# Kernel optimization log

Measured on AMD Instinct MI355X. Metric: run time of the kernel, lower is better.

The kernel has to match this reference:

```python
import jax, jax.numpy as jnp
import numpy as np

N_QUBITS = 14
N_LAYERS = 5
N_ACTIONS = 2
BETA = 1.0
BATCH = 2048
DIM = 2 ** N_QUBITS

# static diagonal sign tables (wire 0 = most significant bit)
_idx = np.arange(DIM)

def _bit(q):
    return (_idx >> (N_QUBITS - 1 - q)) & 1

# CZ ring: all CZ gates are diagonal and commute -> fold into one sign vector
_pairs = [(i, i + 1) for i in range(N_QUBITS - 1)] + ([(N_QUBITS - 1, 0)] if N_QUBITS > 2 else [])
_ring = np.ones(DIM, np.float32)
for _q1, _q2 in _pairs:
    _ring *= np.where((_bit(_q1) & _bit(_q2)) == 1, -1.0, 1.0).astype(np.float32)
RING_SIGN = jnp.asarray(_ring)
# Z tensor Z ... tensor Z eigenvalues: parity of bitstring
_zz = np.where(np.array([bin(i).count('1') for i in range(DIM)]) % 2 == 1, -1.0, 1.0).astype(np.float32)
ZZ_SIGN = jnp.asarray(_zz)


def _rx(t):
    c = jnp.cos(t / 2).astype(jnp.complex64)
    s = (-1j) * jnp.sin(t / 2).astype(jnp.complex64)
    return jnp.stack([jnp.stack([c, s], -1), jnp.stack([s, c], -1)], -2)


def _ry(t):
    c = jnp.cos(t / 2).astype(jnp.complex64)
    s = jnp.sin(t / 2).astype(jnp.complex64)
    return jnp.stack([jnp.stack([c, -s], -1), jnp.stack([s, c], -1)], -2)


def _rz(t):
    em = jnp.exp(-1j * t / 2).astype(jnp.complex64)
    ep = jnp.exp(1j * t / 2).astype(jnp.complex64)
    z = jnp.zeros_like(em)
    return jnp.stack([jnp.stack([em, z], -1), jnp.stack([z, ep], -1)], -2)


def _apply_1q(state, U, q):
    # state: (B, 2^n) complex64; U: (2,2) shared or (B,2,2) per-sample
    B = state.shape[0]
    s = state.reshape(B, 2 ** q, 2, 2 ** (N_QUBITS - q - 1))
    if U.ndim == 2:
        s = jnp.einsum('ij,bljr->blir', U, s)
    else:
        s = jnp.einsum('bij,bljr->blir', U, s)
    return s.reshape(B, DIM)


def _circuit(theta, inp):
    # inp: (B, N_LAYERS * N_QUBITS) encoding angles; returns (B, 1) expval of Z^n
    B = inp.shape[0]
    state = jnp.zeros((B, DIM), jnp.complex64).at[:, 0].set(1.0)
    vi = 0
    for l in range(N_LAYERS + 1):
        ang = theta[vi:vi + 3 * N_QUBITS].reshape(N_QUBITS, 3)
        vi += 3 * N_QUBITS
        for q in range(N_QUBITS):
            # Rx then Ry then Rz fused into one 2x2 unitary
            U = _rz(ang[q, 2]) @ _ry(ang[q, 1]) @ _rx(ang[q, 0])
            state = _apply_1q(state, U, q)
        if l < N_LAYERS:
            state = state * RING_SIGN  # CZ entangling ring
            enc = inp[:, l * N_QUBITS:(l + 1) * N_QUBITS]
            for q in range(N_QUBITS):
                state = _apply_1q(state, _rx(enc[:, q]), q)
    p = state.real ** 2 + state.imag ** 2
    return jnp.sum(p * ZZ_SIGN, axis=1, keepdims=True)


def setup_inputs() -> dict:
    key = jax.random.key(0)
    k1, k2 = jax.random.split(key, 2)
    x = jax.random.normal(k1, (BATCH, N_QUBITS), jnp.float32)
    theta = jax.random.uniform(k2, (3 * N_QUBITS * (N_LAYERS + 1),), jnp.float32) * np.float32(np.pi)
    lam = jnp.ones((N_QUBITS * N_LAYERS,), jnp.float32)
    # Alternating output layer init: [[1, -1, 1, ...]]
    w = jnp.asarray([[(-1.0) ** i for i in range(N_ACTIONS)]], jnp.float32)
    return {"x": x, "theta": theta, "lam": lam, "w": w}


def reference(x, theta, lam, w):
    inp = jnp.tile(x, (1, N_LAYERS)) * lam          # (B, L*n)
    vals = _circuit(theta, inp)                      # (B, 1)
    logits = (vals @ w) * BETA                       # (B, n_actions)
    return jax.nn.softmax(logits, axis=1)
```

## Files before the change

kernel.cpp:

```cpp
#include <hip/hip_runtime.h>
#include <math.h>

#define NQ        14
#define DIM       16384
#define NLAYERS   5
#define NTHREADS  512

typedef float vf2 __attribute__((ext_vector_type(2)));
struct c32 { float x, y; };

__host__ __device__ constexpr int lswz(int i) {
    return i ^ ((i >> 4) & 15) ^ ((i >> 8) & 15) ^ ((i >> 12) & 3);
}
__host__ __device__ constexpr unsigned sjc(int j) {
    return (((j >> 4) & (j >> 3)) ^ ((j >> 3) & (j >> 2)) ^
            ((j >> 2) & (j >> 1)) ^ ((j >> 1) & j)) & 1u;
}
__host__ __device__ constexpr unsigned pjc(int j) {
    return (((j >> 3) & (j >> 2)) ^ ((j >> 2) & (j >> 1)) ^ ((j >> 1) & j)) & 1u;
}

__device__ __forceinline__ c32 cmul(c32 a, c32 b) {
    return { a.x * b.x - a.y * b.y, a.x * b.y + a.y * b.x };
}
__device__ __forceinline__ vf2 sxor(vf2 v, unsigned m) {
    return vf2{ __uint_as_float(__float_as_uint(v.x) ^ m),
                __uint_as_float(__float_as_uint(v.y) ^ m) };
}

__device__ __forceinline__ vf2 cmulv(vf2 g, vf2 z) {
    vf2 o;
    asm("v_pk_mul_f32 %0, %1, %2 op_sel:[1,1] op_sel_hi:[1,0] neg_lo:[0,1] neg_hi:[0,0]\n\t"
        "v_pk_fma_f32 %0, %1, %2, %0 op_sel:[0,0,0] op_sel_hi:[0,1,1]"
        : "=&v"(o) : "v"(g), "v"(z));
    return o;
}

__device__ __forceinline__ void bfr(vf2 r, vf2& A0, vf2& A1) {
    vf2 b0, b1;
    asm("v_pk_mul_f32 %0, %2, %3 op_sel:[0,0] op_sel_hi:[0,1]\n\t"
        "v_pk_fma_f32 %0, %2, %4, %0 op_sel:[1,0,0] op_sel_hi:[1,1,1] neg_lo:[1,0,0] neg_hi:[1,0,0]\n\t"
        "v_pk_mul_f32 %1, %2, %3 op_sel:[1,0] op_sel_hi:[1,1]\n\t"
        "v_pk_fma_f32 %1, %2, %4, %1 op_sel:[0,0,0] op_sel_hi:[0,1,1]"
        : "=&v"(b0), "=&v"(b1)
        : "v"(r), "v"(A0), "v"(A1));
    A0 = b0; A1 = b1;
}

#define APPLY32R(K, RV) { const vf2 rv_ = (RV); _Pragma("unroll") \
    for (int mm = 0; mm < 16; ++mm) { \
        const int r0 = ((mm >> (K)) << ((K) + 1)) | (mm & ((1 << (K)) - 1)); \
        bfr(rv_, a[r0], a[r0 | (1 << (K))]); } }
#define APPLY16R(K, RV) { const vf2 rv_ = (RV); _Pragma("unroll") \
    for (int mm = 0; mm < 8; ++mm) { \
        const int r0 = ((mm >> (K)) << ((K) + 1)) | (mm & ((1 << (K)) - 1)); \
        bfr(rv_, aa[r0], aa[r0 | (1 << (K))]); } }

#define AMASK(j) ((((j) & 1) ? (((j) & 16) ? M11 : M10) : (((j) & 16) ? M01 : M00)) \
                  ^ (sjc(j) << 31))
#define CMASK(v, j) ((((v)) ? (((j) & 8) ? C11 : C10) : (((j) & 8) ? C01 : C00)) \
                     ^ (((pjc(j) ^ ((j) & (v) & 1)) & 1u) << 31))

__device__ __forceinline__ void passB(char* stb, const vf2* GrL, const vf2* Tk, int base2) {
    vf2 a[32];
    #pragma unroll
    for (int j = 0; j < 32; ++j)
        a[j] = *(const vf2*)(stb + (base2 ^ (lswz(j << 4) << 3)));
    #pragma unroll
    for (int j = 0; j < 32; ++j) a[j] = cmulv(Tk[j], a[j]);
    APPLY32R(4, GrL[5]); APPLY32R(3, GrL[6]); APPLY32R(2, GrL[7]);
    APPLY32R(1, GrL[8]); APPLY32R(0, GrL[9]);
    #pragma unroll
    for (int j = 0; j < 32; ++j)
        *(vf2*)(stb + (base2 ^ (lswz(j << 4) << 3))) = a[j];
}

__device__ __forceinline__ void passAA(char* stb, const vf2* GrA, const vf2* GrB,
                                       const vf2* Ta, const vf2* Tb, int base1,
                                       unsigned M00, unsigned M01, unsigned M10, unsigned M11) {
    vf2 a[32];
    #pragma unroll
    for (int j = 0; j < 32; ++j)
        a[j] = *(const vf2*)(stb + (base1 ^ (lswz(j << 9) << 3)));
    #pragma unroll
    for (int j = 0; j < 32; ++j) a[j] = cmulv(Ta[j], a[j]);
    APPLY32R(4, GrA[0]); APPLY32R(3, GrA[1]); APPLY32R(2, GrA[2]);
    APPLY32R(1, GrA[3]); APPLY32R(0, GrA[4]);
    #pragma unroll
    for (int j = 0; j < 32; ++j) a[j] = cmulv(Tb[j], sxor(a[j], AMASK(j)));
    APPLY32R(4, GrB[0]); APPLY32R(3, GrB[1]); APPLY32R(2, GrB[2]);
    APPLY32R(1, GrB[3]); APPLY32R(0, GrB[4]);
    #pragma unroll
    for (int j = 0; j < 32; ++j)
        *(vf2*)(stb + (base1 ^ (lswz(j << 9) << 3))) = a[j];
}

__device__ __forceinline__ void passCC(char* stb, const vf2* GrA, const vf2* GrB,
                                       const vf2* Ta, const vf2* Tb, int base3,
                                       unsigned C00, unsigned C01, unsigned C10, unsigned C11) {
    #pragma unroll
    for (int v = 0; v < 2; ++v) {
        const int bb = base3 ^ (lswz(v << 13) << 3);
        vf2 aa[16];
        #pragma unroll
        for (int j = 0; j < 16; ++j)
            aa[j] = *(const vf2*)(stb + (bb ^ (j << 3)));
        #pragma unroll
        for (int j = 0; j < 16; ++j) aa[j] = cmulv(Ta[j], aa[j]);
        APPLY16R(3, GrA[10]); APPLY16R(2, GrA[11]); APPLY16R(1, GrA[12]); APPLY16R(0, GrA[13]);
        #pragma unroll
        for (int j = 0; j < 16; ++j) aa[j] = cmulv(Tb[j], sxor(aa[j], CMASK(v, j)));
        APPLY16R(3, GrB[10]); APPLY16R(2, GrB[11]); APPLY16R(1, GrB[12]); APPLY16R(0, GrB[13]);
        #pragma unroll
        for (int j = 0; j < 16; ++j)
            *(vf2*)(stb + (bb ^ (j << 3))) = aa[j];
    }
}

__device__ __forceinline__ void passCLast(char* stb, const vf2* GrL, const vf2* Tk,
                                          int base3, float& se, float& so) {
    #pragma unroll
    for (int v = 0; v < 2; ++v) {
        const int bb = base3 ^ (lswz(v << 13) << 3);
        vf2 aa[16];
        #pragma unroll
        for (int j = 0; j < 16; ++j)
            aa[j] = *(const vf2*)(stb + (bb ^ (j << 3)));
        #pragma unroll
        for (int j = 0; j < 16; ++j) aa[j] = cmulv(Tk[j], aa[j]);
        APPLY16R(3, GrL[10]); APPLY16R(2, GrL[11]); APPLY16R(1, GrL[12]); APPLY16R(0, GrL[13]);
        #pragma unroll
        for (int j = 0; j < 16; ++j) {
            const float d = fmaf(aa[j].x, aa[j].x, aa[j].y * aa[j].y);
            if (((v ^ __popc(j)) & 1) == 0) se += d; else so += d;
        }
    }
}

__attribute__((amdgpu_flat_work_group_size(NTHREADS, NTHREADS),
               amdgpu_waves_per_eu(2, 2)))
__global__ void pqc_kernel(
    const float* __restrict__ x,
    const float* __restrict__ theta,
    const float* __restrict__ lam,
    const float* __restrict__ w,
    float* __restrict__ out)
{
    __shared__ vf2 st[DIM];
    __shared__ vf2 Gr[NLAYERS + 1][NQ];
    __shared__ vf2 Gang[NLAYERS + 1][NQ];
    __shared__ vf2 G0c[NQ][2];
    __shared__ vf2 F0[5][2];
    __shared__ vf2 T[15][32];
    __shared__ float wsum[NTHREADS / 64];

    const int t = threadIdx.x;
    const int b = blockIdx.x;
    char* stb = (char*)st;

    if (t < (NLAYERS + 1) * NQ) {
        const int l = t / NQ, q = t % NQ;
        const float a0 = theta[3 * t + 0];
        const float a1 = theta[3 * t + 1];
        const float a2t = theta[3 * t + 2];
        const float cx = cosf(0.5f * a0), sx = sinf(0.5f * a0);
        const float cy = cosf(0.5f * a1), sy = sinf(0.5f * a1);
        const float cz = cosf(0.5f * a2t), sz = sinf(0.5f * a2t);
        const c32 m00 = {  cy * cx,  sy * sx };
        const c32 m01 = { -sy * cx, -cy * sx };
        const c32 m10 = {  sy * cx, -cy * sx };
        c32 u00 = { cz * m00.x + sz * m00.y,  cz * m00.y - sz * m00.x };
        c32 u01 = { cz * m01.x + sz * m01.y,  cz * m01.y - sz * m01.x };
        c32 u10 = { cz * m10.x - sz * m10.y,  cz * m10.y + sz * m10.x };
        if (l >= 1) {
            const float ang = x[b * NQ + q] * lam[(l - 1) * NQ + q];
            const float c = cosf(0.5f * ang), s = sinf(0.5f * ang);
            const c32 u11 = { u00.x, -u00.y };
            const c32 v00 = { u00.x * c + s * u01.y,  u00.y * c - s * u01.x };
            const c32 v10 = { u10.x * c + s * u11.y,  u10.y * c - s * u11.x };
            u00 = v00; u10 = v10;
        }
        if (l == 0) {
            G0c[q][0] = vf2{ u00.x, u00.y };
            G0c[q][1] = vf2{ u10.x, u10.y };
        }
        const float cb = sqrtf(u00.x * u00.x + u00.y * u00.y);
        const float sb = sqrtf(u10.x * u10.x + u10.y * u10.y);
        const float inv = rsqrtf(fmaxf(cb * cb + sb * sb, 1e-30f));
        const float p  = atan2f(u00.y, u00.x);
        const float qq = atan2f(u10.y, u10.x);
        Gr[l][q]   = vf2{ cb * inv, sb * inv };
        Gang[l][q] = vf2{ 0.5f * (qq - p), -0.5f * (p + qq) };
    }
    __syncthreads();

    if (t < 448) {
        const int k = 1 + (t >> 5), j = t & 31;
        const int r = k % 6;
        const int win = (r == 0 || r == 5) ? 0 : ((r == 1 || r == 4) ? 1 : 2);
        if (win != 2 || j < 16) {
            const int lc = 1 + k / 3;
            const int lp = (k >= 3) ? lc - 1 : 0;
            const int nb = (win == 2) ? 4 : 5;
            float th = 0.f;
            for (int m = 0; m < nb; ++m) {
                const int q = (win == 0) ? (4 - m) : (win == 1) ? (9 - m) : (13 - m);
                float ww = Gang[lc][q].y;
                if (lp) ww += Gang[lp][q].x;
                th += ((j >> m) & 1) ? ww : -ww;
            }
            float sn, cn;
            __sincosf(th, &sn, &cn);
            T[k][j] = vf2{ cn, sn };
        }
    } else if (t < 458) {
        const int u = t - 448, q = u >> 1, be = u & 1;
        const float c2 = Gang[1][q].y;
        const float ph = be ? c2 : -c2;
        float sn, cn;
        __sincosf(ph, &sn, &cn);
        const vf2 g = G0c[q][be];
        const c32 f = cmul(c32{ g.x, g.y }, c32{ cn, sn });
        F0[q][be] = vf2{ f.x, f.y };
    }
    __syncthreads();

    const int base1 = lswz(t) << 3;
    const int base2 = lswz(((t & 0x1F0) << 5) | (t & 15)) << 3;
    const int base3 = lswz(t << 4) << 3;
    const unsigned Pp  = (unsigned)(__popc(t & (t >> 1) & 0xFF) & 1);
    const unsigned t8 = (t >> 8) & 1u, tb0 = t & 1u;
    const unsigned M00 =  Pp              << 31;
    const unsigned M10 = (Pp ^ t8)        << 31;
    const unsigned M01 = (Pp ^ tb0)       << 31;
    const unsigned M11 = (Pp ^ t8 ^ tb0)  << 31;
    const unsigned C00 =  Pp              << 31;
    const unsigned C01 = (Pp ^ tb0)       << 31;
    const unsigned C10 = (Pp ^ t8)        << 31;
    const unsigned C11 = (Pp ^ t8 ^ tb0)  << 31;

    {
        c32 pref = { G0c[5][(t >> 8) & 1].x, G0c[5][(t >> 8) & 1].y };
        #pragma unroll
        for (int qq = 6; qq <= 13; ++qq) {
            const vf2 g = G0c[qq][(t >> (13 - qq)) & 1];
            pref = cmul(pref, c32{ g.x, g.y });
        }
        c32 p01p[4], p234[8];
        #pragma unroll
        for (int k = 0; k < 4; ++k) {
            const vf2 ga = F0[0][k >> 1], gb = F0[1][k & 1];
            p01p[k] = cmul(pref, cmul(c32{ ga.x, ga.y }, c32{ gb.x, gb.y }));
        }
        #pragma unroll
        for (int m = 0; m < 8; ++m) {
            const vf2 g2 = F0[2][m >> 2], g3 = F0[3][(m >> 1) & 1], g4 = F0[4][m & 1];
            p234[m] = cmul(cmul(c32{ g2.x, g2.y }, c32{ g3.x, g3.y }), c32{ g4.x, g4.y });
        }
        vf2 a[32];
        #pragma unroll
        for (int j = 0; j < 32; ++j) {
            const c32 av = cmul(p01p[j >> 3], p234[j & 7]);
            a[j] = sxor(vf2{ av.x, av.y }, AMASK(j));
        }
        APPLY32R(4, Gr[1][0]); APPLY32R(3, Gr[1][1]); APPLY32R(2, Gr[1][2]);
        APPLY32R(1, Gr[1][3]); APPLY32R(0, Gr[1][4]);
        #pragma unroll
        for (int j = 0; j < 32; ++j)
            *(vf2*)(stb + (base1 ^ (lswz(j << 9) << 3))) = a[j];
    }
    __syncthreads();

    passB(stb, Gr[1], T[1], base2);                                        __syncthreads();
    passCC(stb, Gr[1], Gr[2], T[2], T[3], base3, C00, C01, C10, C11);      __syncthreads();
    passB(stb, Gr[2], T[4], base2);                                        __syncthreads();
    passAA(stb, Gr[2], Gr[3], T[5], T[6], base1, M00, M01, M10, M11);      __syncthreads();
    passB(stb, Gr[3], T[7], base2);                                        __syncthreads();
    passCC(stb, Gr[3], Gr[4], T[8], T[9], base3, C00, C01, C10, C11);      __syncthreads();
    passB(stb, Gr[4], T[10], base2);                                       __syncthreads();
    passAA(stb, Gr[4], Gr[5], T[11], T[12], base1, M00, M01, M10, M11);    __syncthreads();
    passB(stb, Gr[5], T[13], base2);                                       __syncthreads();
    float se = 0.f, so = 0.f;
    passCLast(stb, Gr[5], T[14], base3, se, so);

    float local = (__popc(t) & 1) ? (so - se) : (se - so);
    #pragma unroll
    for (int off = 32; off > 0; off >>= 1)
        local += __shfl_down(local, off, 64);
    if ((t & 63) == 0) wsum[t >> 6] = local;
    __syncthreads();
    if (t == 0) {
        float v = 0.0f;
        #pragma unroll
        for (int i = 0; i < NTHREADS / 64; ++i) v += wsum[i];
        const float BETA = 1.0f;
        const float l0 = v * w[0] * BETA, l1 = v * w[1] * BETA;
        const float m  = fmaxf(l0, l1);
        const float e0 = __expf(l0 - m), e1 = __expf(l1 - m);
        const float inv = 1.0f / (e0 + e1);
        out[2 * b + 0] = e0 * inv;
        out[2 * b + 1] = e1 * inv;
    }
}

extern "C" void kernel_launch(void* const* d_in, const int* in_sizes, int n_in,
                              void* d_out, int out_size, void* d_ws, size_t ws_size,
                              hipStream_t stream) {
    const float* x     = (const float*)d_in[0];
    const float* theta = (const float*)d_in[1];
    const float* lam   = (const float*)d_in[2];
    const float* w     = (const float*)d_in[3];
    float* out = (float*)d_out;
    const int batch = in_sizes[0] / NQ;
    pqc_kernel<<<batch, NTHREADS, 0, stream>>>(x, theta, lam, w, out);
}
```

Measured before the change: 291.1 us.

## Store LDS statevector in fp16 pairs to halve shared memory and raise occupancy

Stores the 16384-amplitude complex state in shared memory as packed half2 (4 bytes per amplitude) instead of float2, converting to and from fp32 around each pass. The bank swizzle is reworked for 4-byte elements, and waves_per_eu rises from 2 to 4, since halving LDS (128KB to 64KB) allows more blocks per CU. The aim is less LDS traffic and better latency hiding. The cost is fp16 rounding on every pass across many gate layers, which risks accuracy, plus extra conversion instructions and tighter register limits at the higher occupancy.

New measurement: 263.0 us (median of 2 runs). 1.11x faster.

```diff
diff --git a/kernel.cpp b/kernel.cpp
--- a/kernel.cpp
+++ b/kernel.cpp
@@ -1,4 +1,5 @@
 #include <hip/hip_runtime.h>
+#include <hip/hip_fp16.h>
 #include <math.h>
 
 #define NQ        14
@@ -9,8 +10,8 @@
 typedef float vf2 __attribute__((ext_vector_type(2)));
 struct c32 { float x, y; };
 
-__host__ __device__ constexpr int lswz(int i) {
-    return i ^ ((i >> 4) & 15) ^ ((i >> 8) & 15) ^ ((i >> 12) & 3);
+__host__ __device__ constexpr int lswz5(int i) {
+    return i ^ ((i >> 5) & 31) ^ ((i >> 10) & 15);
 }
 __host__ __device__ constexpr unsigned sjc(int j) {
     return (((j >> 4) & (j >> 3)) ^ ((j >> 3) & (j >> 2)) ^
@@ -26,6 +27,16 @@
 __device__ __forceinline__ vf2 sxor(vf2 v, unsigned m) {
     return vf2{ __uint_as_float(__float_as_uint(v.x) ^ m),
                 __uint_as_float(__float_as_uint(v.y) ^ m) };
+}
+
+__device__ __forceinline__ unsigned pk16(vf2 v) {
+    __half2 h = __float22half2_rn(float2{ v.x, v.y });
+    return *reinterpret_cast<unsigned*>(&h);
+}
+__device__ __forceinline__ vf2 up16(unsigned u) {
+    __half2 h = *reinterpret_cast<__half2*>(&u);
+    float2 f = __half22float2(h);
+    return vf2{ f.x, f.y };
 }
 
 __device__ __forceinline__ vf2 cmulv(vf2 g, vf2 z) {
@@ -65,14 +76,14 @@
     vf2 a[32];
     #pragma unroll
     for (int j = 0; j < 32; ++j)
-        a[j] = *(const vf2*)(stb + (base2 ^ (lswz(j << 4) << 3)));
+        a[j] = up16(*(const unsigned*)(stb + (base2 ^ (lswz5(j << 4) << 2))));
     #pragma unroll
     for (int j = 0; j < 32; ++j) a[j] = cmulv(Tk[j], a[j]);
     APPLY32R(4, GrL[5]); APPLY32R(3, GrL[6]); APPLY32R(2, GrL[7]);
     APPLY32R(1, GrL[8]); APPLY32R(0, GrL[9]);
     #pragma unroll
     for (int j = 0; j < 32; ++j)
-        *(vf2*)(stb + (base2 ^ (lswz(j << 4) << 3))) = a[j];
+        *(unsigned*)(stb + (base2 ^ (lswz5(j << 4) << 2))) = pk16(a[j]);
 }
 
 __device__ __forceinline__ void passAA(char* stb, const vf2* GrA, const vf2* GrB,
@@ -81,7 +92,7 @@
     vf2 a[32];
     #pragma unroll
     for (int j = 0; j < 32; ++j)
-        a[j] = *(const vf2*)(stb + (base1 ^ (lswz(j << 9) << 3)));
+        a[j] = up16(*(const unsigned*)(stb + (base1 ^ (lswz5(j << 9) << 2))));
     #pragma unroll
     for (int j = 0; j < 32; ++j) a[j] = cmulv(Ta[j], a[j]);
     APPLY32R(4, GrA[0]); APPLY32R(3, GrA[1]); APPLY32R(2, GrA[2]);
@@ -92,7 +103,7 @@
     APPLY32R(1, GrB[3]); APPLY32R(0, GrB[4]);
     #pragma unroll
     for (int j = 0; j < 32; ++j)
-        *(vf2*)(stb + (base1 ^ (lswz(j << 9) << 3))) = a[j];
+        *(unsigned*)(stb + (base1 ^ (lswz5(j << 9) << 2))) = pk16(a[j]);
 }
 
 __device__ __forceinline__ void passCC(char* stb, const vf2* GrA, const vf2* GrB,
@@ -100,11 +111,11 @@
                                        unsigned C00, unsigned C01, unsigned C10, unsigned C11) {
     #pragma unroll
     for (int v = 0; v < 2; ++v) {
-        const int bb = base3 ^ (lswz(v << 13) << 3);
+        const int bb = base3 ^ (lswz5(v << 13) << 2);
         vf2 aa[16];
         #pragma unroll
         for (int j = 0; j < 16; ++j)
-            aa[j] = *(const vf2*)(stb + (bb ^ (j << 3)));
+            aa[j] = up16(*(const unsigned*)(stb + (bb ^ (j << 2))));
         #pragma unroll
         for (int j = 0; j < 16; ++j) aa[j] = cmulv(Ta[j], aa[j]);
         APPLY16R(3, GrA[10]); APPLY16R(2, GrA[11]); APPLY16R(1, GrA[12]); APPLY16R(0, GrA[13]);
@@ -113,7 +124,7 @@
         APPLY16R(3, GrB[10]); APPLY16R(2, GrB[11]); APPLY16R(1, GrB[12]); APPLY16R(0, GrB[13]);
         #pragma unroll
         for (int j = 0; j < 16; ++j)
-            *(vf2*)(stb + (bb ^ (j << 3))) = aa[j];
+            *(unsigned*)(stb + (bb ^ (j << 2))) = pk16(aa[j]);
     }
 }
 
@@ -121,11 +132,11 @@
                                           int base3, float& se, float& so) {
     #pragma unroll
     for (int v = 0; v < 2; ++v) {
-        const int bb = base3 ^ (lswz(v << 13) << 3);
+        const int bb = base3 ^ (lswz5(v << 13) << 2);
         vf2 aa[16];
         #pragma unroll
         for (int j = 0; j < 16; ++j)
-            aa[j] = *(const vf2*)(stb + (bb ^ (j << 3)));
+            aa[j] = up16(*(const unsigned*)(stb + (bb ^ (j << 2))));
         #pragma unroll
         for (int j = 0; j < 16; ++j) aa[j] = cmulv(Tk[j], aa[j]);
         APPLY16R(3, GrL[10]); APPLY16R(2, GrL[11]); APPLY16R(1, GrL[12]); APPLY16R(0, GrL[13]);
@@ -138,7 +149,7 @@
 }
 
 __attribute__((amdgpu_flat_work_group_size(NTHREADS, NTHREADS),
-               amdgpu_waves_per_eu(2, 2)))
+               amdgpu_waves_per_eu(4, 4)))
 __global__ void pqc_kernel(
     const float* __restrict__ x,
     const float* __restrict__ theta,
@@ -146,7 +157,7 @@
     const float* __restrict__ w,
     float* __restrict__ out)
 {
-    __shared__ vf2 st[DIM];
+    __shared__ unsigned sth[DIM];
     __shared__ vf2 Gr[NLAYERS + 1][NQ];
     __shared__ vf2 Gang[NLAYERS + 1][NQ];
     __shared__ vf2 G0c[NQ][2];
@@ -156,7 +167,7 @@
 
     const int t = threadIdx.x;
     const int b = blockIdx.x;
-    char* stb = (char*)st;
+    char* stb = (char*)sth;
 
     if (t < (NLAYERS + 1) * NQ) {
         const int l = t / NQ, q = t % NQ;
@@ -225,9 +236,9 @@
     }
     __syncthreads();
 
-    const int base1 = lswz(t) << 3;
-    const int base2 = lswz(((t & 0x1F0) << 5) | (t & 15)) << 3;
-    const int base3 = lswz(t << 4) << 3;
+    const int base1 = lswz5(t) << 2;
+    const int base2 = lswz5(((t & 0x1F0) << 5) | (t & 15)) << 2;
+    const int base3 = lswz5(t << 4) << 2;
     const unsigned Pp  = (unsigned)(__popc(t & (t >> 1) & 0xFF) & 1);
     const unsigned t8 = (t >> 8) & 1u, tb0 = t & 1u;
     const unsigned M00 =  Pp              << 31;
@@ -267,7 +278,7 @@
         APPLY32R(1, Gr[1][3]); APPLY32R(0, Gr[1][4]);
         #pragma unroll
         for (int j = 0; j < 32; ++j)
-            *(vf2*)(stb + (base1 ^ (lswz(j << 9) << 3))) = a[j];
+            *(unsigned*)(stb + (base1 ^ (lswz5(j << 9) << 2))) = pk16(a[j]);
     }
     __syncthreads();
 
```
